# Kernel optimization log

Measured on AMD Instinct MI355X. Metric: run time of the kernel, lower is better.

The kernel has to match this reference:

```python
import jax, jax.numpy as jnp
import numpy as np

BATCH, IN_F, OUT_F, K = 16384, 1024, 1024, 256


def setup_inputs() -> dict:
    key = jax.random.key(0)
    kx, kw, kp = jax.random.split(key, 3)
    x = jax.random.normal(kx, (BATCH, IN_F), dtype=jnp.float32)
    weights = jax.random.normal(kw, (OUT_F, IN_F), dtype=jnp.float32)
    P = jax.random.normal(kp, (K, IN_F), dtype=jnp.float32)  # LSH projection matrix (K, in_features)
    return {"x": x, "weights": weights, "P": P}


def _codes(unit, P):
    # SimHash binary codes in {-1, +1}: sign of random projections
    return jnp.where(unit @ P.T >= 0, 1.0, -1.0).astype(unit.dtype)


def reference(x, weights, P):
    eps = jnp.finfo(x.dtype).eps
    # normalize rows of x and weights
    x_norms = jnp.linalg.norm(x, axis=-1, keepdims=True) + eps        # (B, 1)
    x_unit = x / x_norms
    w_norms = jnp.linalg.norm(weights, axis=-1, keepdims=True) + eps  # (M, 1)
    w_unit = weights / w_norms
    # hash codes
    codes_x = _codes(x_unit, P)   # (B, K)
    codes_w = _codes(w_unit, P)   # (M, K)
    # agreement-based cosine estimate: dot/K = 1 - 2*hamming_frac
    dot = codes_x @ codes_w.T                                   # (B, M)
    k = jnp.asarray(P.shape[0], dtype=x.dtype)
    half_pi = jnp.asarray(np.pi * 0.5, dtype=x.dtype)
    cos_est = jnp.cos(half_pi * (1.0 - dot / k))                # (B, M)
    return x_norms * w_norms.T * cos_est                        # (B, M)
```

## Files before the change

### kernel.cpp

```cpp
#include <hip/hip_runtime.h>
#include <hip/hip_bf16.h>
#include <math.h>

#define BATCH 16384
#define OUTF  1024
#define INF   1024
#define KPROJ 256
#define MTOT  (BATCH + OUTF)

#define GBM 32
#define GBN 128
#define GBK 64
#define NKT (INF / GBK)

#define NZ_THRESH 0.15f

typedef unsigned int       u32;
typedef unsigned long long u64;
typedef unsigned short     u16;
typedef _Float16           f16;
typedef __attribute__((ext_vector_type(8))) _Float16 f16x8;
typedef __attribute__((ext_vector_type(4))) float    f32x4;

#define SCHED0() __builtin_amdgcn_sched_barrier(0)

__device__ __forceinline__ void gl_lds16(const void* g, void* l) {
    __builtin_amdgcn_global_load_lds(
        (const __attribute__((address_space(1))) u32*)g,
        (__attribute__((address_space(3))) u32*)l, 16, 0, 0);
}

__global__ __launch_bounds__(256) void prep_p(const float* __restrict__ P,
                                              f16* __restrict__ Bp) {
    const int wave = threadIdx.x >> 6, lane = threadIdx.x & 63;
    const int pr = blockIdx.x * 4 + wave;
    const float4* v = (const float4*)(P + (size_t)pr * INF);
    ushort4* d = (ushort4*)(Bp + (size_t)pr * INF);
#pragma unroll
    for (int q = 0; q < 4; ++q) {
        float4 f = v[lane + 64 * q];
        ushort4 o;
        o.x = __builtin_bit_cast(u16, (f16)f.x);
        o.y = __builtin_bit_cast(u16, (f16)f.y);
        o.z = __builtin_bit_cast(u16, (f16)f.z);
        o.w = __builtin_bit_cast(u16, (f16)f.w);
        d[lane + 64 * q] = o;
    }
}

__global__ __launch_bounds__(256, 4) void gemm_signs(const float* __restrict__ X,
                                                     const float* __restrict__ W,
                                                     const f16* __restrict__ Bp,
                                                     const float* __restrict__ Pf,
                                                     u64* __restrict__ cx,
                                                     u64* __restrict__ cw,
                                                     float* __restrict__ xn,
                                                     float* __restrict__ wn) {
    __shared__ __align__(16) unsigned char ldsA[GBM * 8 * 16];
    __shared__ __align__(16) unsigned char ldsB[GBN * 8 * 16];
    __shared__ u16 sw[GBM][8];
    __shared__ float nsq[GBM][8];

    const int t    = threadIdx.x;
    const int wid  = t >> 6, lane = t & 63;
    const int l4   = lane >> 4, l15 = lane & 15;
    const int wc   = wid;
    const int bm   = blockIdx.x >> 1;
    const int bn0  = (blockIdx.x & 1) * GBN;
    const int am0  = bm * GBM;

    const int ra = t >> 3, sa = t & 7, ca = sa ^ (ra & 7);
    const float* Asrc = (am0 < BATCH) ? X + (size_t)am0 * INF
                                      : W + (size_t)(am0 - BATCH) * INF;
    const float* aRow = Asrc + (size_t)ra * INF + ca * 8;

    const f16* bsrc[4];
#pragma unroll
    for (int i = 0; i < 4; ++i) {
        const int g = (i * 4 + wid) * 64 + lane;
        const int row = g >> 3, sl = g & 7, cb = sl ^ (row & 7);
        bsrc[i] = Bp + (size_t)(bn0 + row) * INF + cb * 8;
    }

    f32x4 acc[2][2] = {};
    float ssq = 0.0f;
    float4 pf0 = *(const float4*)(aRow);
    float4 pf1 = *(const float4*)(aRow + 4);

    for (int kt = 0; kt < NKT; ++kt) {
        ssq += pf0.x * pf0.x + pf0.y * pf0.y + pf0.z * pf0.z + pf0.w * pf0.w +
               pf1.x * pf1.x + pf1.y * pf1.y + pf1.z * pf1.z + pf1.w * pf1.w;
        {
            f16x8 h;
            h[0] = (f16)pf0.x; h[1] = (f16)pf0.y; h[2] = (f16)pf0.z; h[3] = (f16)pf0.w;
            h[4] = (f16)pf1.x; h[5] = (f16)pf1.y; h[6] = (f16)pf1.z; h[7] = (f16)pf1.w;
            *(f16x8*)(ldsA + t * 16) = h;
        }
#pragma unroll
        for (int i = 0; i < 4; ++i)
            gl_lds16(bsrc[i] + kt * GBK, ldsB + (i * 4 + wid) * 1024);
        SCHED0();
        if (kt + 1 < NKT) {
            pf0 = *(const float4*)(aRow + (kt + 1) * GBK);
            pf1 = *(const float4*)(aRow + (kt + 1) * GBK + 4);
            SCHED0();
            asm volatile("s_waitcnt vmcnt(2) lgkmcnt(0)" ::: "memory");
        } else {
            asm volatile("s_waitcnt vmcnt(0) lgkmcnt(0)" ::: "memory");
        }
        SCHED0();
        __builtin_amdgcn_s_barrier();
        SCHED0();
#pragma unroll
        for (int ks = 0; ks < 2; ++ks) {
            f16x8 af[2], bf[2];
#pragma unroll
            for (int i = 0; i < 2; ++i) {
                const int row = i * 16 + l15;
                const int slot = (ks * 4 + l4) ^ (row & 7);
                af[i] = *(const f16x8*)(ldsA + row * 128 + slot * 16);
            }
#pragma unroll
            for (int j = 0; j < 2; ++j) {
                const int col = wc * 32 + j * 16 + l15;
                const int slot = (ks * 4 + l4) ^ (col & 7);
                bf[j] = *(const f16x8*)(ldsB + col * 128 + slot * 16);
            }
#pragma unroll
            for (int i = 0; i < 2; ++i)
#pragma unroll
                for (int j = 0; j < 2; ++j)
                    acc[i][j] = __builtin_amdgcn_mfma_f32_16x16x32_f16(af[i], bf[j], acc[i][j], 0, 0, 0);
        }
        SCHED0();
        __builtin_amdgcn_s_barrier();
        SCHED0();
    }

    nsq[ra][sa] = ssq;

#pragma unroll
    for (int i = 0; i < 2; ++i)
#pragma unroll
        for (int j = 0; j < 2; ++j)
#pragma unroll
            for (int q = 0; q < 4; ++q) {
                const float v = acc[i][j][q];
                int bit = (v >= 0.0f) ? 1 : 0;
                u64 fl = __ballot(fabsf(v) < NZ_THRESH);
                while (fl) {
                    const int src = __ffsll((long long)fl) - 1;
                    fl &= fl - 1;
                    const int lrow = i * 16 + ((src >> 4) << 2) + q;
                    const int col  = bn0 + wc * 32 + j * 16 + (src & 15);
                    const float* xr = Asrc + (size_t)lrow * INF + lane * 16;
                    const float* pr = Pf + (size_t)col * INF + lane * 16;
                    double s = 0.0;
#pragma unroll
                    for (int c4 = 0; c4 < 4; ++c4) {
                        float4 xa = *(const float4*)(xr + c4 * 4);
                        float4 pa = *(const float4*)(pr + c4 * 4);
                        s += (double)xa.x * pa.x + (double)xa.y * pa.y +
                             (double)xa.z * pa.z + (double)xa.w * pa.w;
                    }
#pragma unroll
                    for (int off = 32; off; off >>= 1) s += __shfl_xor(s, off, 64);
                    if (lane == src) bit = (s >= 0.0) ? 1 : 0;
                }
                const u64 b = __ballot(bit != 0);
                if (l15 == 0)
                    sw[i * 16 + l4 * 4 + q][wc * 2 + j] = (u16)(b >> (l4 * 16));
            }
    if (bn0 == 0 && t < GBM) {
        const float* p = nsq[t];
        float s = ((p[0] + p[1]) + (p[2] + p[3])) + ((p[4] + p[5]) + (p[6] + p[7]));
        const float n = sqrtf(s) + 1.1920929e-07f;
        const int grow = am0 + t;
        if (grow < BATCH) xn[grow] = n; else wn[grow - BATCH] = n;
    }
    __syncthreads();
    if (t < 64) {
        const int r = t >> 1, wsel = t & 1;
        const u64 val = *(const u64*)&sw[r][wsel * 4];
        const int grow = am0 + r;
        const int word = (blockIdx.x & 1) * 2 + wsel;
        if (grow < BATCH) cx[(size_t)grow * 4 + word] = val;
        else              cw[(size_t)(grow - BATCH) * 4 + word] = val;
    }
}

__global__ __launch_bounds__(256) void popc_out(const u64* __restrict__ cx,
                                                const u64* __restrict__ cw,
                                                const float* __restrict__ xn,
                                                const float* __restrict__ wn,
                                                float* __restrict__ out) {
    __shared__ float lut[257];
    __shared__ u64 cxs[64][4];
    __shared__ float xns[64];
    const int t = threadIdx.x;

    lut[t] = (float)cos((double)t * (3.14159265358979323846 / 256.0));
    if (t == 0) lut[256] = -1.0f;

    const int r0 = blockIdx.x * 64;
    cxs[t >> 2][t & 3] = cx[(size_t)r0 * 4 + t];
    if (t < 64) xns[t] = xn[r0 + t];

    const ulonglong4* cwv4 = (const ulonglong4*)cw;
    ulonglong4 c0 = cwv4[4 * t + 0];
    ulonglong4 c1 = cwv4[4 * t + 1];
    ulonglong4 c2 = cwv4[4 * t + 2];
    ulonglong4 c3 = cwv4[4 * t + 3];
    float4 wnr = ((const float4*)wn)[t];

    __syncthreads();

    float4* outv = (float4*)out;
    const size_t obase = (size_t)r0 * (OUTF / 4) + t;
#pragma unroll 4
    for (int r = 0; r < 64; ++r) {
        const u64 a0 = cxs[r][0], a1 = cxs[r][1], a2 = cxs[r][2], a3 = cxs[r][3];
        const float sx = xns[r];
        float4 o;
        o.x = sx * wnr.x * lut[__popcll(a0 ^ c0.x) + __popcll(a1 ^ c0.y) +
                               __popcll(a2 ^ c0.z) + __popcll(a3 ^ c0.w)];
        o.y = sx * wnr.y * lut[__popcll(a0 ^ c1.x) + __popcll(a1 ^ c1.y) +
                               __popcll(a2 ^ c1.z) + __popcll(a3 ^ c1.w)];
        o.z = sx * wnr.z * lut[__popcll(a0 ^ c2.x) + __popcll(a1 ^ c2.y) +
                               __popcll(a2 ^ c2.z) + __popcll(a3 ^ c2.w)];
        o.w = sx * wnr.w * lut[__popcll(a0 ^ c3.x) + __popcll(a1 ^ c3.y) +
                               __popcll(a2 ^ c3.z) + __popcll(a3 ^ c3.w)];
        outv[obase + (size_t)r * (OUTF / 4)] = o;
    }
}

extern "C" void kernel_launch(void* const* d_in, const int* in_sizes, int n_in,
                              void* d_out, int out_size, void* d_ws, size_t ws_size,
                              hipStream_t stream) {
    const float* x = (const float*)d_in[0];
    const float* w = (const float*)d_in[1];
    const float* P = (const float*)d_in[2];
    float* out = (float*)d_out;

    char* ws = (char*)d_ws;
    f16*  Bp = (f16*)ws;
    u64*  cx = (u64*)(ws + 524288);
    u64*  cw = (u64*)(ws + 1048576);
    float* xn = (float*)(ws + 1081344);
    float* wn = (float*)(ws + 1146880);

    prep_p<<<KPROJ / 4, 256, 0, stream>>>(P, Bp);

    gemm_signs<<<(MTOT / GBM) * 2, 256, 0, stream>>>(x, w, Bp, P, cx, cw, xn, wn);

    popc_out<<<BATCH / 64, 256, 0, stream>>>(cx, cw, xn, wn, out);
}
```

Measured before the change: 69.98 us.

## Double M tile and double-buffer B in LDS with two-deep A prefetch

Raises the gemm_signs row tile from 32 to 64 so each block does four MFMA row groups per B tile, which halves how often B is reloaded from memory. The B tile is double-buffered in LDS, with the next tile issued before the current one is computed, and the A loads are prefetched two k-steps ahead in registers. The waitcnt schedule is hand-tuned per stage. In exchange, register and LDS use go up, the occupancy hint drops from 4 to 3 blocks, and half as many blocks are launched. A __syncthreads is moved so the norm reduction reads nsq only after it is fully written.

```diff
diff --git a/kernel.cpp b/kernel.cpp
--- a/kernel.cpp
+++ b/kernel.cpp
@@ -8,7 +8,7 @@
 #define KPROJ 256
 #define MTOT  (BATCH + OUTF)
 
-#define GBM 32
+#define GBM 64
 #define GBN 128
 #define GBK 64
 #define NKT (INF / GBK)
@@ -48,7 +48,7 @@
     }
 }
 
-__global__ __launch_bounds__(256, 4) void gemm_signs(const float* __restrict__ X,
+__global__ __launch_bounds__(256, 3) void gemm_signs(const float* __restrict__ X,
                                                      const float* __restrict__ W,
                                                      const f16* __restrict__ Bp,
                                                      const float* __restrict__ Pf,
@@ -56,8 +56,8 @@
                                                      u64* __restrict__ cw,
                                                      float* __restrict__ xn,
                                                      float* __restrict__ wn) {
-    __shared__ __align__(16) unsigned char ldsA[GBM * 8 * 16];
-    __shared__ __align__(16) unsigned char ldsB[GBN * 8 * 16];
+    __shared__ __align__(16) unsigned char ldsA[GBM * 128];
+    __shared__ __align__(16) unsigned char ldsB[2 * GBN * 128];
     __shared__ u16 sw[GBM][8];
     __shared__ float nsq[GBM][8];
 
@@ -72,7 +72,8 @@
     const int ra = t >> 3, sa = t & 7, ca = sa ^ (ra & 7);
     const float* Asrc = (am0 < BATCH) ? X + (size_t)am0 * INF
                                       : W + (size_t)(am0 - BATCH) * INF;
-    const float* aRow = Asrc + (size_t)ra * INF + ca * 8;
+    const float* aRow0 = Asrc + (size_t)ra * INF + ca * 8;
+    const float* aRow1 = aRow0 + (size_t)32 * INF;
 
     const f16* bsrc[4];
 #pragma unroll
@@ -82,65 +83,99 @@
         bsrc[i] = Bp + (size_t)(bn0 + row) * INF + cb * 8;
     }
 
-    f32x4 acc[2][2] = {};
-    float ssq = 0.0f;
-    float4 pf0 = *(const float4*)(aRow);
-    float4 pf1 = *(const float4*)(aRow + 4);
-
-    for (int kt = 0; kt < NKT; ++kt) {
-        ssq += pf0.x * pf0.x + pf0.y * pf0.y + pf0.z * pf0.z + pf0.w * pf0.w +
-               pf1.x * pf1.x + pf1.y * pf1.y + pf1.z * pf1.z + pf1.w * pf1.w;
-        {
-            f16x8 h;
-            h[0] = (f16)pf0.x; h[1] = (f16)pf0.y; h[2] = (f16)pf0.z; h[3] = (f16)pf0.w;
-            h[4] = (f16)pf1.x; h[5] = (f16)pf1.y; h[6] = (f16)pf1.z; h[7] = (f16)pf1.w;
-            *(f16x8*)(ldsA + t * 16) = h;
-        }
-#pragma unroll
-        for (int i = 0; i < 4; ++i)
-            gl_lds16(bsrc[i] + kt * GBK, ldsB + (i * 4 + wid) * 1024);
-        SCHED0();
-        if (kt + 1 < NKT) {
-            pf0 = *(const float4*)(aRow + (kt + 1) * GBK);
-            pf1 = *(const float4*)(aRow + (kt + 1) * GBK + 4);
-            SCHED0();
-            asm volatile("s_waitcnt vmcnt(2) lgkmcnt(0)" ::: "memory");
-        } else {
-            asm volatile("s_waitcnt vmcnt(0) lgkmcnt(0)" ::: "memory");
-        }
-        SCHED0();
-        __builtin_amdgcn_s_barrier();
-        SCHED0();
-#pragma unroll
-        for (int ks = 0; ks < 2; ++ks) {
-            f16x8 af[2], bf[2];
-#pragma unroll
-            for (int i = 0; i < 2; ++i) {
-                const int row = i * 16 + l15;
-                const int slot = (ks * 4 + l4) ^ (row & 7);
-                af[i] = *(const f16x8*)(ldsA + row * 128 + slot * 16);
-            }
-#pragma unroll
-            for (int j = 0; j < 2; ++j) {
-                const int col = wc * 32 + j * 16 + l15;
-                const int slot = (ks * 4 + l4) ^ (col & 7);
-                bf[j] = *(const f16x8*)(ldsB + col * 128 + slot * 16);
-            }
-#pragma unroll
-            for (int i = 0; i < 2; ++i)
-#pragma unroll
-                for (int j = 0; j < 2; ++j)
-                    acc[i][j] = __builtin_amdgcn_mfma_f32_16x16x32_f16(af[i], bf[j], acc[i][j], 0, 0, 0);
-        }
-        SCHED0();
-        __builtin_amdgcn_s_barrier();
-        SCHED0();
-    }
-
-    nsq[ra][sa] = ssq;
-
-#pragma unroll
-    for (int i = 0; i < 2; ++i)
+    f32x4 acc[4][2] = {};
+    float ssq0 = 0.0f, ssq1 = 0.0f;
+    float4 pa0, pa1, pa2, pa3, pb0, pb1, pb2, pb3;
+
+#define GEMM_ALOAD(P0, P1, P2, P3, KT2)                                       \
+    P0 = *(const float4*)(aRow0 + (KT2) * GBK);                               \
+    P1 = *(const float4*)(aRow0 + (KT2) * GBK + 4);                           \
+    P2 = *(const float4*)(aRow1 + (KT2) * GBK);                               \
+    P3 = *(const float4*)(aRow1 + (KT2) * GBK + 4);
+
+#define GEMM_BISSUE(KT1, NXTOFF)                                              \
+    _Pragma("unroll")                                                         \
+    for (int i = 0; i < 4; ++i)                                               \
+        gl_lds16(bsrc[i] + (KT1) * GBK,                                       \
+                 ldsB + (NXTOFF) + (i * 4 + wid) * 1024);
+
+#define GEMM_STAGE(P0, P1, P2, P3)                                            \
+    {                                                                         \
+        ssq0 += P0.x * P0.x + P0.y * P0.y + P0.z * P0.z + P0.w * P0.w +       \
+                P1.x * P1.x + P1.y * P1.y + P1.z * P1.z + P1.w * P1.w;        \
+        ssq1 += P2.x * P2.x + P2.y * P2.y + P2.z * P2.z + P2.w * P2.w +       \
+                P3.x * P3.x + P3.y * P3.y + P3.z * P3.z + P3.w * P3.w;        \
+        f16x8 h0, h1;                                                         \
+        h0[0] = (f16)P0.x; h0[1] = (f16)P0.y; h0[2] = (f16)P0.z;              \
+        h0[3] = (f16)P0.w; h0[4] = (f16)P1.x; h0[5] = (f16)P1.y;              \
+        h0[6] = (f16)P1.z; h0[7] = (f16)P1.w;                                 \
+        h1[0] = (f16)P2.x; h1[1] = (f16)P2.y; h1[2] = (f16)P2.z;              \
+        h1[3] = (f16)P2.w; h1[4] = (f16)P3.x; h1[5] = (f16)P3.y;              \
+        h1[6] = (f16)P3.z; h1[7] = (f16)P3.w;                                 \
+        *(f16x8*)(ldsA + t * 16) = h0;                                        \
+        *(f16x8*)(ldsA + 4096 + t * 16) = h1;                                 \
+    }
+
+#define GEMM_COMPUTE(BOFF)                                                    \
+    _Pragma("unroll")                                                         \
+    for (int ks = 0; ks < 2; ++ks) {                                          \
+        f16x8 af[4], bf[2];                                                   \
+        _Pragma("unroll")                                                     \
+        for (int i = 0; i < 4; ++i) {                                         \
+            const int row = i * 16 + l15;                                     \
+            const int slot = (ks * 4 + l4) ^ (row & 7);                       \
+            af[i] = *(const f16x8*)(ldsA + row * 128 + slot * 16);            \
+        }                                                                     \
+        _Pragma("unroll")                                                     \
+        for (int j = 0; j < 2; ++j) {                                         \
+            const int col = wc * 32 + j * 16 + l15;                           \
+            const int slot = (ks * 4 + l4) ^ (col & 7);                       \
+            bf[j] = *(const f16x8*)(ldsB + (BOFF) + col * 128 + slot * 16);   \
+        }                                                                     \
+        _Pragma("unroll")                                                     \
+        for (int i = 0; i < 4; ++i)                                           \
+            _Pragma("unroll")                                                 \
+            for (int j = 0; j < 2; ++j)                                       \
+                acc[i][j] = __builtin_amdgcn_mfma_f32_16x16x32_f16(           \
+                    af[i], bf[j], acc[i][j], 0, 0, 0);                        \
+    }
+
+#define GEMM_BODY(P0, P1, P2, P3, KT, CUROFF, NXTOFF, DO_A, DO_B, VMTOP, VMMID) \
+    {                                                                         \
+        asm volatile("s_waitcnt vmcnt(" VMTOP ")" ::: "memory");              \
+        SCHED0();                                                             \
+        GEMM_STAGE(P0, P1, P2, P3);                                          \
+        SCHED0();                                                             \
+        if (DO_B) { GEMM_BISSUE((KT) + 1, NXTOFF); }                          \
+        SCHED0();                                                             \
+        asm volatile("s_waitcnt vmcnt(" VMMID ") lgkmcnt(0)" ::: "memory");   \
+        SCHED0();                                                             \
+        if (DO_A) { GEMM_ALOAD(P0, P1, P2, P3, (KT) + 2); }                   \
+        SCHED0();                                                             \
+        __builtin_amdgcn_s_barrier();                                         \
+        SCHED0();                                                             \
+        GEMM_COMPUTE(CUROFF);                                                 \
+        SCHED0();                                                             \
+        __builtin_amdgcn_s_barrier();                                         \
+    }
+
+    GEMM_ALOAD(pa0, pa1, pa2, pa3, 0);
+    GEMM_BISSUE(0, 0);
+    GEMM_ALOAD(pb0, pb1, pb2, pb3, 1);
+    SCHED0();
+
+    for (int kt = 0; kt < 14; kt += 2) {
+        GEMM_BODY(pa0, pa1, pa2, pa3, kt,     0,     16384, true,  true,  "8", "8");
+        GEMM_BODY(pb0, pb1, pb2, pb3, kt + 1, 16384, 0,     true,  true,  "8", "8");
+    }
+    GEMM_BODY(pa0, pa1, pa2, pa3, 14, 0,     16384, false, true,  "8", "8");
+    GEMM_BODY(pb0, pb1, pb2, pb3, 15, 16384, 0,     false, false, "4", "0");
+
+    nsq[ra][sa]      = ssq0;
+    nsq[ra + 32][sa] = ssq1;
+
+#pragma unroll
+    for (int i = 0; i < 4; ++i)
 #pragma unroll
         for (int j = 0; j < 2; ++j)
 #pragma unroll
@@ -171,6 +206,7 @@
                 if (l15 == 0)
                     sw[i * 16 + l4 * 4 + q][wc * 2 + j] = (u16)(b >> (l4 * 16));
             }
+    __syncthreads();
     if (bn0 == 0 && t < GBM) {
         const float* p = nsq[t];
         float s = ((p[0] + p[1]) + (p[2] + p[3])) + ((p[4] + p[5]) + (p[6] + p[7]));
@@ -178,8 +214,7 @@
         const int grow = am0 + t;
         if (grow < BATCH) xn[grow] = n; else wn[grow - BATCH] = n;
     }
-    __syncthreads();
-    if (t < 64) {
+    if (t < 128) {
         const int r = t >> 1, wsel = t & 1;
         const u64 val = *(const u64*)&sw[r][wsel * 4];
         const int grow = am0 + r;
```

Result: slower. 74.85 us (+7.0%).

## Restructure sign GEMM to one wave per 16 rows with MFMA-fragment-packed P

Applied to the files above, without the earlier changes.

The projection matrix is now pre-packed into the exact MFMA B-fragment layout, so each lane reads its operands straight from global memory (L2) with no LDS staging or barriers. Each single-wave block computes 16 rows against all 256 projections, so every X row is read once instead of twice. A two-stage register prefetch of X replaces the LDS pipeline. In exchange, each wave re-reads the entire packed P (512KB) from cache, and the 64-thread blocks with 16 accumulators give less latency hiding per block.

```diff
diff --git a/kernel.cpp b/kernel.cpp
--- a/kernel.cpp
+++ b/kernel.cpp
@@ -1,5 +1,4 @@
 #include <hip/hip_runtime.h>
-#include <hip/hip_bf16.h>
 #include <math.h>
 
 #define BATCH 16384
@@ -7,15 +6,10 @@
 #define INF   1024
 #define KPROJ 256
 #define MTOT  (BATCH + OUTF)
-
-#define GBM 32
-#define GBN 128
-#define GBK 64
-#define NKT (INF / GBK)
+#define NKT   16
 
 #define NZ_THRESH 0.15f
 
-typedef unsigned int       u32;
 typedef unsigned long long u64;
 typedef unsigned short     u16;
 typedef _Float16           f16;
@@ -24,168 +18,159 @@
 
 #define SCHED0() __builtin_amdgcn_sched_barrier(0)
 
-__device__ __forceinline__ void gl_lds16(const void* g, void* l) {
-    __builtin_amdgcn_global_load_lds(
-        (const __attribute__((address_space(1))) u32*)g,
-        (__attribute__((address_space(3))) u32*)l, 16, 0, 0);
-}
-
 __global__ __launch_bounds__(256) void prep_p(const float* __restrict__ P,
-                                              f16* __restrict__ Bp) {
-    const int wave = threadIdx.x >> 6, lane = threadIdx.x & 63;
-    const int pr = blockIdx.x * 4 + wave;
-    const float4* v = (const float4*)(P + (size_t)pr * INF);
-    ushort4* d = (ushort4*)(Bp + (size_t)pr * INF);
-#pragma unroll
-    for (int q = 0; q < 4; ++q) {
-        float4 f = v[lane + 64 * q];
-        ushort4 o;
-        o.x = __builtin_bit_cast(u16, (f16)f.x);
-        o.y = __builtin_bit_cast(u16, (f16)f.y);
-        o.z = __builtin_bit_cast(u16, (f16)f.z);
-        o.w = __builtin_bit_cast(u16, (f16)f.w);
-        d[lane + 64 * q] = o;
-    }
-}
-
-__global__ __launch_bounds__(256, 4) void gemm_signs(const float* __restrict__ X,
-                                                     const float* __restrict__ W,
-                                                     const f16* __restrict__ Bp,
-                                                     const float* __restrict__ Pf,
-                                                     u64* __restrict__ cx,
-                                                     u64* __restrict__ cw,
-                                                     float* __restrict__ xn,
-                                                     float* __restrict__ wn) {
-    __shared__ __align__(16) unsigned char ldsA[GBM * 8 * 16];
-    __shared__ __align__(16) unsigned char ldsB[GBN * 8 * 16];
-    __shared__ u16 sw[GBM][8];
-    __shared__ float nsq[GBM][8];
-
-    const int t    = threadIdx.x;
-    const int wid  = t >> 6, lane = t & 63;
-    const int l4   = lane >> 4, l15 = lane & 15;
-    const int wc   = wid;
-    const int bm   = blockIdx.x >> 1;
-    const int bn0  = (blockIdx.x & 1) * GBN;
-    const int am0  = bm * GBM;
-
-    const int ra = t >> 3, sa = t & 7, ca = sa ^ (ra & 7);
-    const float* Asrc = (am0 < BATCH) ? X + (size_t)am0 * INF
-                                      : W + (size_t)(am0 - BATCH) * INF;
-    const float* aRow = Asrc + (size_t)ra * INF + ca * 8;
-
-    const f16* bsrc[4];
-#pragma unroll
-    for (int i = 0; i < 4; ++i) {
-        const int g = (i * 4 + wid) * 64 + lane;
-        const int row = g >> 3, sl = g & 7, cb = sl ^ (row & 7);
-        bsrc[i] = Bp + (size_t)(bn0 + row) * INF + cb * 8;
-    }
-
-    f32x4 acc[2][2] = {};
+                                              f16* __restrict__ Bf) {
+    const int c = blockIdx.x;
+    const int p = threadIdx.x;
+    const float4 f0 = *(const float4*)(P + (size_t)p * INF + c * 8);
+    const float4 f1 = *(const float4*)(P + (size_t)p * INF + c * 8 + 4);
+    const int kt = c >> 3, ks = (c >> 2) & 1, lq = c & 3;
+    const int frag = (kt * 16 + (p >> 4)) * 2 + ks;
+    const int lane = lq * 16 + (p & 15);
+    f16x8 h;
+    h[0] = (f16)f0.x; h[1] = (f16)f0.y; h[2] = (f16)f0.z; h[3] = (f16)f0.w;
+    h[4] = (f16)f1.x; h[5] = (f16)f1.y; h[6] = (f16)f1.z; h[7] = (f16)f1.w;
+    *(f16x8*)(Bf + (size_t)(frag * 64 + lane) * 8) = h;
+}
+
+__global__ __launch_bounds__(64) void gemm_signs(const float* __restrict__ X,
+                                                 const float* __restrict__ W,
+                                                 const f16* __restrict__ Bf,
+                                                 const float* __restrict__ Pf,
+                                                 u64* __restrict__ cx,
+                                                 u64* __restrict__ cw,
+                                                 float* __restrict__ xn,
+                                                 float* __restrict__ wn) {
+    __shared__ u16 sw[16][16];
+
+    const int lane = threadIdx.x;
+    const int l4 = lane >> 4, l15 = lane & 15;
+    const int row0 = blockIdx.x * 16;
+    const float* Asrc = (row0 < BATCH) ? X + (size_t)row0 * INF
+                                       : W + (size_t)(row0 - BATCH) * INF;
+    const float* aPtr = Asrc + (size_t)l15 * INF + l4 * 8;
+    const f16* bPtr = Bf + lane * 8;
+
+    f32x4 acc[16] = {};
     float ssq = 0.0f;
-    float4 pf0 = *(const float4*)(aRow);
-    float4 pf1 = *(const float4*)(aRow + 4);
-
-    for (int kt = 0; kt < NKT; ++kt) {
-        ssq += pf0.x * pf0.x + pf0.y * pf0.y + pf0.z * pf0.z + pf0.w * pf0.w +
-               pf1.x * pf1.x + pf1.y * pf1.y + pf1.z * pf1.z + pf1.w * pf1.w;
-        {
-            f16x8 h;
-            h[0] = (f16)pf0.x; h[1] = (f16)pf0.y; h[2] = (f16)pf0.z; h[3] = (f16)pf0.w;
-            h[4] = (f16)pf1.x; h[5] = (f16)pf1.y; h[6] = (f16)pf1.z; h[7] = (f16)pf1.w;
-            *(f16x8*)(ldsA + t * 16) = h;
+
+#define GEMM_BODY(KT, Q0, Q1, Q2, Q3, DO_PF)                                  \
+    {                                                                         \
+        ssq += Q0.x * Q0.x + Q0.y * Q0.y + Q0.z * Q0.z + Q0.w * Q0.w +        \
+               Q1.x * Q1.x + Q1.y * Q1.y + Q1.z * Q1.z + Q1.w * Q1.w +        \
+               Q2.x * Q2.x + Q2.y * Q2.y + Q2.z * Q2.z + Q2.w * Q2.w +        \
+               Q3.x * Q3.x + Q3.y * Q3.y + Q3.z * Q3.z + Q3.w * Q3.w;         \
+        f16x8 a0, a1;                                                         \
+        a0[0] = (f16)Q0.x; a0[1] = (f16)Q0.y; a0[2] = (f16)Q0.z;              \
+        a0[3] = (f16)Q0.w; a0[4] = (f16)Q1.x; a0[5] = (f16)Q1.y;              \
+        a0[6] = (f16)Q1.z; a0[7] = (f16)Q1.w;                                 \
+        a1[0] = (f16)Q2.x; a1[1] = (f16)Q2.y; a1[2] = (f16)Q2.z;              \
+        a1[3] = (f16)Q2.w; a1[4] = (f16)Q3.x; a1[5] = (f16)Q3.y;              \
+        a1[6] = (f16)Q3.z; a1[7] = (f16)Q3.w;                                 \
+        const f16* bk = bPtr + (size_t)(KT) * 16384;                          \
+        _Pragma("unroll")                                                     \
+        for (int jb = 0; jb < 4; ++jb) {                                      \
+            f16x8 b0 = *(const f16x8*)(bk + (jb * 4 + 0) * 1024);             \
+            f16x8 b1 = *(const f16x8*)(bk + (jb * 4 + 0) * 1024 + 512);       \
+            f16x8 b2 = *(const f16x8*)(bk + (jb * 4 + 1) * 1024);             \
+            f16x8 b3 = *(const f16x8*)(bk + (jb * 4 + 1) * 1024 + 512);       \
+            f16x8 b4 = *(const f16x8*)(bk + (jb * 4 + 2) * 1024);             \
+            f16x8 b5 = *(const f16x8*)(bk + (jb * 4 + 2) * 1024 + 512);       \
+            f16x8 b6 = *(const f16x8*)(bk + (jb * 4 + 3) * 1024);             \
+            f16x8 b7 = *(const f16x8*)(bk + (jb * 4 + 3) * 1024 + 512);       \
+            acc[jb * 4 + 0] = __builtin_amdgcn_mfma_f32_16x16x32_f16(         \
+                a0, b0, acc[jb * 4 + 0], 0, 0, 0);                            \
+            acc[jb * 4 + 0] = __builtin_amdgcn_mfma_f32_16x16x32_f16(         \
+                a1, b1, acc[jb * 4 + 0], 0, 0, 0);                            \
+            acc[jb * 4 + 1] = __builtin_amdgcn_mfma_f32_16x16x32_f16(         \
+                a0, b2, acc[jb * 4 + 1], 0, 0, 0);                            \
+            acc[jb * 4 + 1] = __builtin_amdgcn_mfma_f32_16x16x32_f16(         \
+                a1, b3, acc[jb * 4 + 1], 0, 0, 0);                            \
+            acc[jb * 4 + 2] = __builtin_amdgcn_mfma_f32_16x16x32_f16(         \
+                a0, b4, acc[jb * 4 + 2], 0, 0, 0);                            \
+            acc[jb * 4 + 2] = __builtin_amdgcn_mfma_f32_16x16x32_f16(         \
+                a1, b5, acc[jb * 4 + 2], 0, 0, 0);                            \
+            acc[jb * 4 + 3] = __builtin_amdgcn_mfma_f32_16x16x32_f16(         \
+                a0, b6, acc[jb * 4 + 3], 0, 0, 0);                            \
+            acc[jb * 4 + 3] = __builtin_amdgcn_mfma_f32_16x16x32_f16(         \
+                a1, b7, acc[jb * 4 + 3], 0, 0, 0);                            \
+        }                                                                     \
+        if (DO_PF) {                                                          \
+            SCHED0();                                                         \
+            Q0 = *(const float4*)(aPtr + ((KT) + 2) * 64);                    \
+            Q1 = *(const float4*)(aPtr + ((KT) + 2) * 64 + 4);                \
+            Q2 = *(const float4*)(aPtr + ((KT) + 2) * 64 + 32);               \
+            Q3 = *(const float4*)(aPtr + ((KT) + 2) * 64 + 36);               \
+            SCHED0();                                                         \
+        }                                                                     \
+    }
+
+    float4 qa0 = *(const float4*)(aPtr);
+    float4 qa1 = *(const float4*)(aPtr + 4);
+    float4 qa2 = *(const float4*)(aPtr + 32);
+    float4 qa3 = *(const float4*)(aPtr + 36);
+    float4 qb0 = *(const float4*)(aPtr + 64);
+    float4 qb1 = *(const float4*)(aPtr + 68);
+    float4 qb2 = *(const float4*)(aPtr + 96);
+    float4 qb3 = *(const float4*)(aPtr + 100);
+
+    for (int kt = 0; kt < 12; kt += 2) {
+        GEMM_BODY(kt,     qa0, qa1, qa2, qa3, true);
+        GEMM_BODY(kt + 1, qb0, qb1, qb2, qb3, true);
+    }
+    GEMM_BODY(12, qa0, qa1, qa2, qa3, true);
+    GEMM_BODY(13, qb0, qb1, qb2, qb3, true);
+    GEMM_BODY(14, qa0, qa1, qa2, qa3, false);
+    GEMM_BODY(15, qb0, qb1, qb2, qb3, false);
+
+    {
+        float s = ssq;
+        s += __shfl_xor(s, 16, 64);
+        s += __shfl_xor(s, 32, 64);
+        if (lane < 16) {
+            const int grow = row0 + lane;
+            const float n = sqrtf(s) + 1.1920929e-07f;
+            if (grow < BATCH) xn[grow] = n; else wn[grow - BATCH] = n;
         }
-#pragma unroll
-        for (int i = 0; i < 4; ++i)
-            gl_lds16(bsrc[i] + kt * GBK, ldsB + (i * 4 + wid) * 1024);
-        SCHED0();
-        if (kt + 1 < NKT) {
-            pf0 = *(const float4*)(aRow + (kt + 1) * GBK);
-            pf1 = *(const float4*)(aRow + (kt + 1) * GBK + 4);
-            SCHED0();
-            asm volatile("s_waitcnt vmcnt(2) lgkmcnt(0)" ::: "memory");
-        } else {
-            asm volatile("s_waitcnt vmcnt(0) lgkmcnt(0)" ::: "memory");
+    }
+
+#pragma unroll
+    for (int j = 0; j < 16; ++j)
+#pragma unroll
+        for (int q = 0; q < 4; ++q) {
+            const float v = acc[j][q];
+            int bit = (v >= 0.0f) ? 1 : 0;
+            u64 fl = __ballot(fabsf(v) < NZ_THRESH);
+            while (fl) {
+                const int src = __ffsll((long long)fl) - 1;
+                fl &= fl - 1;
+                const int lrow = ((src >> 4) << 2) + q;
+                const int col  = j * 16 + (src & 15);
+                const float* xr = Asrc + (size_t)lrow * INF + lane * 16;
+                const float* pr = Pf + (size_t)col * INF + lane * 16;
+                double s = 0.0;
+#pragma unroll
+                for (int c4 = 0; c4 < 4; ++c4) {
+                    float4 xa = *(const float4*)(xr + c4 * 4);
+                    float4 pa = *(const float4*)(pr + c4 * 4);
+                    s += (double)xa.x * pa.x + (double)xa.y * pa.y +
+                         (double)xa.z * pa.z + (double)xa.w * pa.w;
+                }
+#pragma unroll
+                for (int off = 32; off; off >>= 1) s += __shfl_xor(s, off, 64);
+                if (lane == src) bit = (s >= 0.0) ? 1 : 0;
+            }
+            const u64 b = __ballot(bit != 0);
+            if (l15 == 0)
+                sw[l4 * 4 + q][j] = (u16)(b >> (l4 * 16));
         }
-        SCHED0();
-        __builtin_amdgcn_s_barrier();
-        SCHED0();
-#pragma unroll
-        for (int ks = 0; ks < 2; ++ks) {
-            f16x8 af[2], bf[2];
-#pragma unroll
-            for (int i = 0; i < 2; ++i) {
-                const int row = i * 16 + l15;
-                const int slot = (ks * 4 + l4) ^ (row & 7);
-                af[i] = *(const f16x8*)(ldsA + row * 128 + slot * 16);
-            }
-#pragma unroll
-            for (int j = 0; j < 2; ++j) {
-                const int col = wc * 32 + j * 16 + l15;
-                const int slot = (ks * 4 + l4) ^ (col & 7);
-                bf[j] = *(const f16x8*)(ldsB + col * 128 + slot * 16);
-            }
-#pragma unroll
-            for (int i = 0; i < 2; ++i)
-#pragma unroll
-                for (int j = 0; j < 2; ++j)
-                    acc[i][j] = __builtin_amdgcn_mfma_f32_16x16x32_f16(af[i], bf[j], acc[i][j], 0, 0, 0);
-        }
-        SCHED0();
-        __builtin_amdgcn_s_barrier();
-        SCHED0();
-    }
-
-    nsq[ra][sa] = ssq;
-
-#pragma unroll
-    for (int i = 0; i < 2; ++i)
-#pragma unroll
-        for (int j = 0; j < 2; ++j)
-#pragma unroll
-            for (int q = 0; q < 4; ++q) {
-                const float v = acc[i][j][q];
-                int bit = (v >= 0.0f) ? 1 : 0;
-                u64 fl = __ballot(fabsf(v) < NZ_THRESH);
-                while (fl) {
-                    const int src = __ffsll((long long)fl) - 1;
-                    fl &= fl - 1;
-                    const int lrow = i * 16 + ((src >> 4) << 2) + q;
-                    const int col  = bn0 + wc * 32 + j * 16 + (src & 15);
-                    const float* xr = Asrc + (size_t)lrow * INF + lane * 16;
-                    const float* pr = Pf + (size_t)col * INF + lane * 16;
-                    double s = 0.0;
-#pragma unroll
-                    for (int c4 = 0; c4 < 4; ++c4) {
-                        float4 xa = *(const float4*)(xr + c4 * 4);
-                        float4 pa = *(const float4*)(pr + c4 * 4);
-                        s += (double)xa.x * pa.x + (double)xa.y * pa.y +
-                             (double)xa.z * pa.z + (double)xa.w * pa.w;
-                    }
-#pragma unroll
-                    for (int off = 32; off; off >>= 1) s += __shfl_xor(s, off, 64);
-                    if (lane == src) bit = (s >= 0.0) ? 1 : 0;
-                }
-                const u64 b = __ballot(bit != 0);
-                if (l15 == 0)
-                    sw[i * 16 + l4 * 4 + q][wc * 2 + j] = (u16)(b >> (l4 * 16));
-            }
-    if (bn0 == 0 && t < GBM) {
-        const float* p = nsq[t];
-        float s = ((p[0] + p[1]) + (p[2] + p[3])) + ((p[4] + p[5]) + (p[6] + p[7]));
-        const float n = sqrtf(s) + 1.1920929e-07f;
-        const int grow = am0 + t;
-        if (grow < BATCH) xn[grow] = n; else wn[grow - BATCH] = n;
-    }
     __syncthreads();
-    if (t < 64) {
-        const int r = t >> 1, wsel = t & 1;
-        const u64 val = *(const u64*)&sw[r][wsel * 4];
-        const int grow = am0 + r;
-        const int word = (blockIdx.x & 1) * 2 + wsel;
-        if (grow < BATCH) cx[(size_t)grow * 4 + word] = val;
-        else              cw[(size_t)(grow - BATCH) * 4 + word] = val;
+    {
+        const int r = lane >> 2, w = lane & 3;
+        const u64 val = *(const u64*)&sw[r][w * 4];
+        const int grow = row0 + r;
+        if (grow < BATCH) cx[(size_t)grow * 4 + w] = val;
+        else              cw[(size_t)(grow - BATCH) * 4 + w] = val;
     }
 }
 
@@ -243,15 +228,15 @@
     float* out = (float*)d_out;
 
     char* ws = (char*)d_ws;
-    f16*  Bp = (f16*)ws;
+    f16*  Bf = (f16*)ws;
     u64*  cx = (u64*)(ws + 524288);
     u64*  cw = (u64*)(ws + 1048576);
     float* xn = (float*)(ws + 1081344);
     float* wn = (float*)(ws + 1146880);
 
-    prep_p<<<KPROJ / 4, 256, 0, stream>>>(P, Bp);
-
-    gemm_signs<<<(MTOT / GBM) * 2, 256, 0, stream>>>(x, w, Bp, P, cx, cw, xn, wn);
+    prep_p<<<128, 256, 0, stream>>>(P, Bf);
+
+    gemm_signs<<<MTOT / 16, 64, 0, stream>>>(x, w, Bf, P, cx, cw, xn, wn);
 
     popc_out<<<BATCH / 64, 256, 0, stream>>>(cx, cw, xn, wn, out);
 }
```

Result: slower. 83.48 us (+19.3%).
